# Kernel optimization log

Measured on AMD Instinct MI355X. Metric: run time of the kernel, lower is better.

## Reference

```python
import jax, jax.numpy as jnp
import numpy as np

N = 262144
FC = 256
XYZ_FREQ, DIR_FREQ = 10, 4
IN_XYZ = 3 + 3 * 2 * XYZ_FREQ  # 63
IN_DIR = 3 + 3 * 2 * DIR_FREQ  # 27
SKIP = 4


def posenc(p, n_freqs):
    bands = 2.0 ** jnp.arange(n_freqs, dtype=p.dtype)          # [F]
    xb = p[..., None, :] * bands[:, None]                       # [N, F, 3]
    sc = jnp.stack([jnp.sin(xb), jnp.cos(xb)], axis=-2)         # [N, F, 2, 3]
    return jnp.concatenate([p, sc.reshape(p.shape[0], n_freqs * 6)], axis=-1)


def setup_inputs() -> dict:
    key = jax.random.key(0)
    ks = jax.random.split(key, 32)
    s = 0.05
    inp = {"x": jax.random.normal(ks[0], (N, 6), jnp.float32)}
    dims_in = [IN_XYZ] + [FC + IN_XYZ if i == SKIP else FC for i in range(1, 8)]
    for i in range(8):
        inp[f"w{i}"] = jax.random.normal(ks[1 + i], (dims_in[i], FC), jnp.float32) * s
        inp[f"b{i}"] = jnp.zeros((FC,), jnp.float32)
    inp["w_final"] = jax.random.normal(ks[10], (FC, FC), jnp.float32) * s
    inp["b_final"] = jnp.zeros((FC,), jnp.float32)
    inp["w_sigma"] = jax.random.normal(ks[11], (FC, 1), jnp.float32) * s
    inp["b_sigma"] = jnp.zeros((1,), jnp.float32)
    inp["w_rgb1"] = jax.random.normal(ks[12], (FC + IN_DIR, FC // 2), jnp.float32) * s
    inp["b_rgb1"] = jnp.zeros((FC // 2,), jnp.float32)
    inp["w_rgb2"] = jax.random.normal(ks[13], (FC // 2, 3), jnp.float32) * s
    inp["b_rgb2"] = jnp.zeros((3,), jnp.float32)
    return inp


def reference(x, w0, b0, w1, b1, w2, b2, w3, b3, w4, b4, w5, b5, w6, b6, w7, b7,
              w_final, b_final, w_sigma, b_sigma, w_rgb1, b_rgb1, w_rgb2, b_rgb2):
    input_xyz = posenc(x[:, :3], XYZ_FREQ)   # [N, 63]
    input_dir = posenc(x[:, 3:], DIR_FREQ)   # [N, 27]
    ws = [w0, w1, w2, w3, w4, w5, w6, w7]
    bs = [b0, b1, b2, b3, b4, b5, b6, b7]
    h = input_xyz
    for i in range(8):
        if i == SKIP:
            h = jnp.concatenate([input_xyz, h], axis=-1)
        h = jax.nn.relu(h @ ws[i] + bs[i])
    sigma = h @ w_sigma + b_sigma                               # [N, 1]
    final = h @ w_final + b_final                               # [N, 256]
    dir_enc = jnp.concatenate([final, input_dir], axis=-1)      # [N, 283]
    hidden = jax.nn.relu(dir_enc @ w_rgb1 + b_rgb1)
    rgb = jax.nn.sigmoid(hidden @ w_rgb2 + b_rgb2)              # [N, 3]
    return jnp.concatenate([rgb, sigma], axis=-1)               # [N, 4]
```

## Files before the change

### kernel.cpp

```cpp
#include <hip/hip_runtime.h>
#include <hip/hip_fp16.h>
#include <stdint.h>

typedef unsigned int   uint32;
typedef unsigned short ushort_t;
typedef _Float16 half8   __attribute__((ext_vector_type(8)));
typedef float    floatx4 __attribute__((ext_vector_type(4)));

#define DEVINL __device__ __forceinline__

#define N_FRAGS 1172

DEVINL int fragoff(int row, int f) {
    return (f >> 5)*2048 + (row >> 4)*512 + ((f >> 3) & 3)*128 + (row & 15)*8 + (f & 7);
}

__device__ __align__(16) ushort_t g_ws[(size_t)N_FRAGS * 512];

DEVINL ushort_t f2h_u(float v) { return __half_as_ushort(__float2half(v)); }

DEVINL uint32 pk_relu(uint32 a) {
    uint32 r;
    asm("v_pk_max_f16 %0, %1, 0" : "=v"(r) : "v"(a));
    return r;
}

DEVINL void fast_sincos(float v, float& s, float& c) {
    float t = v * 0.15915494f;
    t = t - floorf(t);
    s = __builtin_amdgcn_sinf(t);
    c = __builtin_amdgcn_cosf(t);
}

__global__ __launch_bounds__(256) void prep_weights(
    const float* __restrict__ w0, const float* __restrict__ w1,
    const float* __restrict__ w2, const float* __restrict__ w3,
    const float* __restrict__ w4, const float* __restrict__ w5,
    const float* __restrict__ w6, const float* __restrict__ w7,
    const float* __restrict__ wf, const float* __restrict__ wsig,
    const float* __restrict__ wr1, const float* __restrict__ wr2)
{
    const int frag = blockIdx.x;
    const int w    = threadIdx.x;
    const int l    = w >> 2;
    const int jj   = w & 3;
    const int q = l >> 4, cc = l & 15;

    constexpr int foff[13] = {0,32,160,288,416,576,704,832,960,1088,1096,1168,1172};
    int t = 0;
    #pragma unroll
    for (int i = 1; i <= 11; ++i) if (frag >= foff[i]) t = i;

    const float* W; int fo, ntc, Kr, Nr;
    switch (t) {
        case 0:  W = w0;   fo = 0;    ntc = 16; Kr = 63;  Nr = 256; break;
        case 1:  W = w1;   fo = 32;   ntc = 16; Kr = 256; Nr = 256; break;
        case 2:  W = w2;   fo = 160;  ntc = 16; Kr = 256; Nr = 256; break;
        case 3:  W = w3;   fo = 288;  ntc = 16; Kr = 256; Nr = 256; break;
        case 4:  W = w4;   fo = 416;  ntc = 16; Kr = 319; Nr = 256; break;
        case 5:  W = w5;   fo = 576;  ntc = 16; Kr = 256; Nr = 256; break;
        case 6:  W = w6;   fo = 704;  ntc = 16; Kr = 256; Nr = 256; break;
        case 7:  W = w7;   fo = 832;  ntc = 16; Kr = 256; Nr = 256; break;
        case 8:  W = wf;   fo = 960;  ntc = 16; Kr = 256; Nr = 256; break;
        case 9:  W = wsig; fo = 1088; ntc = 1;  Kr = 256; Nr = 1;   break;
        case 10: W = wr1;  fo = 1096; ntc = 8;  Kr = 283; Nr = 128; break;
        default: W = wr2;  fo = 1168; ntc = 1;  Kr = 128; Nr = 3;   break;
    }
    const int skip63 = (t == 4);
    const int fl = frag - fo;
    const int nt = fl % ntc;
    const int kt = fl / ntc;
    const int n  = nt*16 + cc;

    ushort_t h2[2];
    #pragma unroll
    for (int e = 0; e < 2; ++e) {
        const int k = kt*32 + q*8 + jj*2 + e;
        float v = 0.f;
        if (n < Nr) {
            if (skip63) {
                if (k != 63) { const int rr = (k < 63) ? k : (k - 1); v = W[(size_t)rr*Nr + n]; }
            } else if (k < Kr) {
                v = W[(size_t)k*Nr + n];
            }
        }
        h2[e] = f2h_u(v);
    }
    const uint32 pk = (uint32)h2[0] | ((uint32)h2[1] << 16);
    ((uint32*)(g_ws + (size_t)frag*512))[l*4 + jj] = pk;
}

template <int NT_W, int KT, int KT_SPLIT, int NTT>
DEVINL void run_layer(const ushort_t* __restrict__ wsrc,
                      const ushort_t* __restrict__ in0,
                      const ushort_t* __restrict__ in1,
                      int lane, int nt_lo,
                      const floatx4 (&binit)[NT_W], floatx4 (&acc)[4][NT_W])
{
    half8 bfr[2][4];
    half8 afr[2][NT_W];

    const ushort_t* ap  = wsrc + (size_t)nt_lo*512 + (size_t)lane*8;
    const ushort_t* b0p = in0 + lane*8;
    const ushort_t* b1p = in1 + lane*8;

    auto loadA = [&](int kt, int buf) {
        const ushort_t* p = ap + (size_t)kt*NTT*512;
        #pragma unroll
        for (int nt = 0; nt < NT_W; ++nt)
            afr[buf][nt] = *(const half8*)(p + nt*512);
    };
    auto loadB = [&](int kt, int buf) {
        const ushort_t* bb = (kt < KT_SPLIT) ? b0p + kt*2048
                                             : b1p + (kt - KT_SPLIT)*2048;
        #pragma unroll
        for (int rt = 0; rt < 4; ++rt)
            bfr[buf][rt] = *(const half8*)(bb + rt*512);
    };

    loadA(0, 0);
    loadB(0, 0);
    #pragma unroll
    for (int kt = 0; kt < KT; ++kt) {
        const int cur = kt & 1;
        if (kt + 1 < KT) { loadA(kt + 1, cur ^ 1); loadB(kt + 1, cur ^ 1); }
        __builtin_amdgcn_s_setprio(1);
        #pragma unroll
        for (int nt = 0; nt < NT_W; ++nt)
            #pragma unroll
            for (int rt = 0; rt < 4; ++rt)
                acc[rt][nt] = __builtin_amdgcn_mfma_f32_16x16x32_f16(
                    afr[cur][nt], bfr[cur][rt],
                    (kt == 0) ? binit[nt] : acc[rt][nt], 0, 0, 0);
        __builtin_amdgcn_s_setprio(0);
    }
}

template <int NT_W, bool RELU>
DEVINL void epilogue_h(floatx4 (&acc)[4][NT_W], int nt_lo,
                       ushort_t* __restrict__ dsth, int q, int cc)
{
    ushort_t* base = dsth + (nt_lo >> 1)*2048 + (q >> 1)*128 + cc*8 + (q & 1)*4;
    #pragma unroll
    for (int rt = 0; rt < 4; ++rt) {
        #pragma unroll
        for (int nt = 0; nt < NT_W; ++nt) {
            const floatx4 v = acc[rt][nt];
            uint2 u;
            u.x = __builtin_bit_cast(uint32, __builtin_amdgcn_cvt_pkrtz(v.x, v.y));
            u.y = __builtin_bit_cast(uint32, __builtin_amdgcn_cvt_pkrtz(v.z, v.w));
            if (RELU) {
                u.x = pk_relu(u.x);
                u.y = pk_relu(u.y);
            }
            const int coff = (nt >> 1)*2048 + ((2*nt) & 3)*128 + rt*512;
            *(uint2*)(base + coff) = u;
        }
    }
}

__global__ __launch_bounds__(256, 3) void nerf_fused(
    const float* __restrict__ x,
    const float* __restrict__ b0, const float* __restrict__ b1,
    const float* __restrict__ b2, const float* __restrict__ b3,
    const float* __restrict__ b4, const float* __restrict__ b5,
    const float* __restrict__ b6, const float* __restrict__ b7,
    const float* __restrict__ bf, const float* __restrict__ bsig,
    const float* __restrict__ br1, const float* __restrict__ br2,
    float* __restrict__ out)
{
    __shared__ __align__(16) ushort_t shh[8*2048];
    __shared__ __align__(16) ushort_t shx[2*2048];
    __shared__ __align__(16) ushort_t shd[2048];

    const int tid  = threadIdx.x;
    const int wave = tid >> 6, lane = tid & 63;
    const int q = lane >> 4, cc = lane & 15;
    const int r0 = blockIdx.x * 64;
    const ushort_t* ws = g_ws;

    {
        const int r = lane;
        const float* xr = x + (size_t)(r0 + r)*6;
        for (int j = wave; j < 42; j += 4) {
            float s, c;
            if (j < 30) {
                int f = j/3, a = j%3;
                fast_sincos(xr[a] * (float)(1 << f), s, c);
                shx[fragoff(r, 3 + f*6 + a)]     = f2h_u(s);
                shx[fragoff(r, 3 + f*6 + 3 + a)] = f2h_u(c);
            } else {
                int jj = j - 30, f = jj/3, a = jj%3;
                fast_sincos(xr[3+a] * (float)(1 << f), s, c);
                shd[fragoff(r, 3 + f*6 + a)]     = f2h_u(s);
                shd[fragoff(r, 3 + f*6 + 3 + a)] = f2h_u(c);
            }
        }
        if (wave == 0) {
            #pragma unroll
            for (int a = 0; a < 3; ++a) {
                shx[fragoff(r, a)] = f2h_u(xr[a]);
                shd[fragoff(r, a)] = f2h_u(xr[3+a]);
            }
            shx[fragoff(r, 63)] = 0;
            #pragma unroll
            for (int kq = 27; kq < 32; ++kq) shd[fragoff(r, kq)] = 0;
        }
    }
    __syncthreads();

    const float* BS[8] = {b0,b1,b2,b3,b4,b5,b6,b7};
    const int WO[8] = {0,16384,81920,147456,212992,294912,360448,425984};
    const int nt_lo4 = wave * 4;
    const floatx4 vz = {0.f, 0.f, 0.f, 0.f};

    floatx4 acc[4][4];
    floatx4 bl[4];

    #pragma unroll
    for (int nt = 0; nt < 4; ++nt)
        bl[nt] = *(const floatx4*)(b0 + (nt_lo4 + nt)*16 + q*4);
    run_layer<4,2,2,16>(ws + WO[0], shx, shx, lane, nt_lo4, bl, acc);
    epilogue_h<4,true>(acc, nt_lo4, shh, q, cc);
    __syncthreads();

    #pragma unroll
    for (int l = 1; l < 8; ++l) {
        #pragma unroll
        for (int nt = 0; nt < 4; ++nt)
            bl[nt] = *(const floatx4*)(BS[l] + (nt_lo4 + nt)*16 + q*4);
        if (l == 4)
            run_layer<4,10,2,16>(ws + WO[4], shx, shh, lane, nt_lo4, bl, acc);
        else
            run_layer<4,8,8,16>(ws + WO[l], shh, shh, lane, nt_lo4, bl, acc);
        __syncthreads();
        epilogue_h<4,true>(acc, nt_lo4, shh, q, cc);
        __syncthreads();
    }

    if (wave == 0) {
        floatx4 sacc[4][1];
        const floatx4 bz[1] = {vz};
        run_layer<1,8,8,1>(ws + 557056, shh, shh, lane, 0, bz, sacc);
        if (q == 0) {
            const float bs_ = bsig[0];
            #pragma unroll
            for (int rt = 0; rt < 4; ++rt)
                out[(size_t)(r0 + rt*16 + cc)*4 + 3] = sacc[rt][0].x + bs_;
        }
    }

    #pragma unroll
    for (int nt = 0; nt < 4; ++nt)
        bl[nt] = *(const floatx4*)(bf + (nt_lo4 + nt)*16 + q*4);
    run_layer<4,8,8,16>(ws + 491520, shh, shh, lane, nt_lo4, bl, acc);
    __syncthreads();
    epilogue_h<4,false>(acc, nt_lo4, shh, q, cc);
    __syncthreads();

    {
        floatx4 racc[4][2];
        floatx4 bl2[2];
        #pragma unroll
        for (int nt = 0; nt < 2; ++nt)
            bl2[nt] = *(const floatx4*)(br1 + (wave*2 + nt)*16 + q*4);
        run_layer<2,9,8,8>(ws + 561152, shh, shd, lane, wave*2, bl2, racc);
        __syncthreads();
        epilogue_h<2,true>(racc, wave*2, shh, q, cc);
        __syncthreads();
    }

    if (wave == 0) {
        floatx4 cacc[4][1];
        const floatx4 bz[1] = {vz};
        run_layer<1,4,4,1>(ws + 598016, shh, shh, lane, 0, bz, cacc);
        if (q == 0) {
            const float c0 = br2[0], c1 = br2[1], c2 = br2[2];
            #pragma unroll
            for (int rt = 0; rt < 4; ++rt) {
                const size_t o = (size_t)(r0 + rt*16 + cc)*4;
                out[o+0] = 1.f/(1.f + __expf(-(cacc[rt][0].x + c0)));
                out[o+1] = 1.f/(1.f + __expf(-(cacc[rt][0].y + c1)));
                out[o+2] = 1.f/(1.f + __expf(-(cacc[rt][0].z + c2)));
            }
        }
    }
}

extern "C" void kernel_launch(void* const* d_in, const int* in_sizes, int n_in,
                              void* d_out, int out_size, void* d_ws, size_t ws_size,
                              hipStream_t stream)
{
    const float* x  = (const float*)d_in[0];
    const float* w0 = (const float*)d_in[1];  const float* b0 = (const float*)d_in[2];
    const float* w1 = (const float*)d_in[3];  const float* b1 = (const float*)d_in[4];
    const float* w2 = (const float*)d_in[5];  const float* b2 = (const float*)d_in[6];
    const float* w3 = (const float*)d_in[7];  const float* b3 = (const float*)d_in[8];
    const float* w4 = (const float*)d_in[9];  const float* b4 = (const float*)d_in[10];
    const float* w5 = (const float*)d_in[11]; const float* b5 = (const float*)d_in[12];
    const float* w6 = (const float*)d_in[13]; const float* b6 = (const float*)d_in[14];
    const float* w7 = (const float*)d_in[15]; const float* b7 = (const float*)d_in[16];
    const float* wf = (const float*)d_in[17]; const float* bf = (const float*)d_in[18];
    const float* wsg= (const float*)d_in[19]; const float* bsg= (const float*)d_in[20];
    const float* wr1= (const float*)d_in[21]; const float* br1= (const float*)d_in[22];
    const float* wr2= (const float*)d_in[23]; const float* br2= (const float*)d_in[24];
    float* out = (float*)d_out;
    const int N = in_sizes[0] / 6;

    prep_weights<<<N_FRAGS, 256, 0, stream>>>(
        w0,w1,w2,w3,w4,w5,w6,w7,wf,wsg,wr1,wr2);
    nerf_fused<<<N/64, 256, 0, stream>>>(
        x, b0,b1,b2,b3,b4,b5,b6,b7, bf,bsg, br1,br2, out);
}
```

Measured before the change: 365.5 us.

## Split each 64-row tile across 8 waves with two row groups

Doubles the block to 512 threads so that each wave computes 32 rows by 64 output columns instead of 64 by 64. This halves the accumulator registers per wave and should allow more waves in flight. The rgb1 layer is redistributed to give one 16-column tile per wave, and the epilogue gains a single-tile addressing path. The cost is that each weight fragment is now loaded from global memory by two waves instead of one, and block-wide barriers now synchronize 8 waves.

```diff
diff --git a/kernel.cpp b/kernel.cpp
--- a/kernel.cpp
+++ b/kernel.cpp
@@ -90,14 +90,14 @@
     ((uint32*)(g_ws + (size_t)frag*512))[l*4 + jj] = pk;
 }
 
-template <int NT_W, int KT, int KT_SPLIT, int NTT>
+template <int RT, int NT_W, int KT, int KT_SPLIT, int NTT>
 DEVINL void run_layer(const ushort_t* __restrict__ wsrc,
                       const ushort_t* __restrict__ in0,
                       const ushort_t* __restrict__ in1,
                       int lane, int nt_lo,
-                      const floatx4 (&binit)[NT_W], floatx4 (&acc)[4][NT_W])
-{
-    half8 bfr[2][4];
+                      const floatx4 (&binit)[NT_W], floatx4 (&acc)[RT][NT_W])
+{
+    half8 bfr[2][RT];
     half8 afr[2][NT_W];
 
     const ushort_t* ap  = wsrc + (size_t)nt_lo*512 + (size_t)lane*8;
@@ -114,7 +114,7 @@
         const ushort_t* bb = (kt < KT_SPLIT) ? b0p + kt*2048
                                              : b1p + (kt - KT_SPLIT)*2048;
         #pragma unroll
-        for (int rt = 0; rt < 4; ++rt)
+        for (int rt = 0; rt < RT; ++rt)
             bfr[buf][rt] = *(const half8*)(bb + rt*512);
     };
 
@@ -128,7 +128,7 @@
         #pragma unroll
         for (int nt = 0; nt < NT_W; ++nt)
             #pragma unroll
-            for (int rt = 0; rt < 4; ++rt)
+            for (int rt = 0; rt < RT; ++rt)
                 acc[rt][nt] = __builtin_amdgcn_mfma_f32_16x16x32_f16(
                     afr[cur][nt], bfr[cur][rt],
                     (kt == 0) ? binit[nt] : acc[rt][nt], 0, 0, 0);
@@ -136,13 +136,12 @@
     }
 }
 
-template <int NT_W, bool RELU>
-DEVINL void epilogue_h(floatx4 (&acc)[4][NT_W], int nt_lo,
+template <int RT, int NT_W, bool RELU>
+DEVINL void epilogue_h(floatx4 (&acc)[RT][NT_W], int nt_lo,
                        ushort_t* __restrict__ dsth, int q, int cc)
 {
-    ushort_t* base = dsth + (nt_lo >> 1)*2048 + (q >> 1)*128 + cc*8 + (q & 1)*4;
-    #pragma unroll
-    for (int rt = 0; rt < 4; ++rt) {
+    #pragma unroll
+    for (int rt = 0; rt < RT; ++rt) {
         #pragma unroll
         for (int nt = 0; nt < NT_W; ++nt) {
             const floatx4 v = acc[rt][nt];
@@ -153,13 +152,21 @@
                 u.x = pk_relu(u.x);
                 u.y = pk_relu(u.y);
             }
-            const int coff = (nt >> 1)*2048 + ((2*nt) & 3)*128 + rt*512;
-            *(uint2*)(base + coff) = u;
-        }
-    }
-}
-
-__global__ __launch_bounds__(256, 3) void nerf_fused(
+            int dst;
+            if constexpr (NT_W > 1) {
+                dst = (nt_lo >> 1)*2048 + (q >> 1)*128 + cc*8 + (q & 1)*4
+                    + (nt >> 1)*2048 + ((2*nt) & 3)*128 + rt*512;
+            } else {
+                const int ng = nt_lo + nt;
+                dst = (ng >> 1)*2048 + rt*512
+                    + (((2*ng + (q >> 1)) & 3)*16 + cc)*8 + (q & 1)*4;
+            }
+            *(uint2*)(dsth + dst) = u;
+        }
+    }
+}
+
+__global__ __launch_bounds__(512, 4) void nerf_fused(
     const float* __restrict__ x,
     const float* __restrict__ b0, const float* __restrict__ b1,
     const float* __restrict__ b2, const float* __restrict__ b3,
@@ -179,10 +186,15 @@
     const int r0 = blockIdx.x * 64;
     const ushort_t* ws = g_ws;
 
+    const int w4 = wave & 3;
+    const int rg = wave >> 2;
+    const int rgo = rg * 1024;
+    const int nt_lo4 = w4 * 4;
+
     {
         const int r = lane;
         const float* xr = x + (size_t)(r0 + r)*6;
-        for (int j = wave; j < 42; j += 4) {
+        for (int j = wave; j < 42; j += 8) {
             float s, c;
             if (j < 30) {
                 int f = j/3, a = j%3;
@@ -211,17 +223,16 @@
 
     const float* BS[8] = {b0,b1,b2,b3,b4,b5,b6,b7};
     const int WO[8] = {0,16384,81920,147456,212992,294912,360448,425984};
-    const int nt_lo4 = wave * 4;
     const floatx4 vz = {0.f, 0.f, 0.f, 0.f};
 
-    floatx4 acc[4][4];
+    floatx4 acc[2][4];
     floatx4 bl[4];
 
     #pragma unroll
     for (int nt = 0; nt < 4; ++nt)
         bl[nt] = *(const floatx4*)(b0 + (nt_lo4 + nt)*16 + q*4);
-    run_layer<4,2,2,16>(ws + WO[0], shx, shx, lane, nt_lo4, bl, acc);
-    epilogue_h<4,true>(acc, nt_lo4, shh, q, cc);
+    run_layer<2,4,2,2,16>(ws + WO[0], shx + rgo, shx + rgo, lane, nt_lo4, bl, acc);
+    epilogue_h<2,4,true>(acc, nt_lo4, shh + rgo, q, cc);
     __syncthreads();
 
     #pragma unroll
@@ -230,18 +241,18 @@
         for (int nt = 0; nt < 4; ++nt)
             bl[nt] = *(const floatx4*)(BS[l] + (nt_lo4 + nt)*16 + q*4);
         if (l == 4)
-            run_layer<4,10,2,16>(ws + WO[4], shx, shh, lane, nt_lo4, bl, acc);
+            run_layer<2,4,10,2,16>(ws + WO[4], shx + rgo, shh + rgo, lane, nt_lo4, bl, acc);
         else
-            run_layer<4,8,8,16>(ws + WO[l], shh, shh, lane, nt_lo4, bl, acc);
+            run_layer<2,4,8,8,16>(ws + WO[l], shh + rgo, shh + rgo, lane, nt_lo4, bl, acc);
         __syncthreads();
-        epilogue_h<4,true>(acc, nt_lo4, shh, q, cc);
+        epilogue_h<2,4,true>(acc, nt_lo4, shh + rgo, q, cc);
         __syncthreads();
     }
 
     if (wave == 0) {
         floatx4 sacc[4][1];
         const floatx4 bz[1] = {vz};
-        run_layer<1,8,8,1>(ws + 557056, shh, shh, lane, 0, bz, sacc);
+        run_layer<4,1,8,8,1>(ws + 557056, shh, shh, lane, 0, bz, sacc);
         if (q == 0) {
             const float bs_ = bsig[0];
             #pragma unroll
@@ -253,27 +264,25 @@
     #pragma unroll
     for (int nt = 0; nt < 4; ++nt)
         bl[nt] = *(const floatx4*)(bf + (nt_lo4 + nt)*16 + q*4);
-    run_layer<4,8,8,16>(ws + 491520, shh, shh, lane, nt_lo4, bl, acc);
+    run_layer<2,4,8,8,16>(ws + 491520, shh + rgo, shh + rgo, lane, nt_lo4, bl, acc);
     __syncthreads();
-    epilogue_h<4,false>(acc, nt_lo4, shh, q, cc);
+    epilogue_h<2,4,false>(acc, nt_lo4, shh + rgo, q, cc);
     __syncthreads();
 
     {
-        floatx4 racc[4][2];
-        floatx4 bl2[2];
-        #pragma unroll
-        for (int nt = 0; nt < 2; ++nt)
-            bl2[nt] = *(const floatx4*)(br1 + (wave*2 + nt)*16 + q*4);
-        run_layer<2,9,8,8>(ws + 561152, shh, shd, lane, wave*2, bl2, racc);
+        floatx4 racc[4][1];
+        floatx4 bl2[1];
+        bl2[0] = *(const floatx4*)(br1 + wave*16 + q*4);
+        run_layer<4,1,9,8,8>(ws + 561152, shh, shd, lane, wave, bl2, racc);
         __syncthreads();
-        epilogue_h<2,true>(racc, wave*2, shh, q, cc);
+        epilogue_h<4,1,true>(racc, wave, shh, q, cc);
         __syncthreads();
     }
 
     if (wave == 0) {
         floatx4 cacc[4][1];
         const floatx4 bz[1] = {vz};
-        run_layer<1,4,4,1>(ws + 598016, shh, shh, lane, 0, bz, cacc);
+        run_layer<4,1,4,4,1>(ws + 598016, shh, shh, lane, 0, bz, cacc);
         if (q == 0) {
             const float c0 = br2[0], c1 = br2[1], c2 = br2[2];
             #pragma unroll
@@ -309,6 +318,6 @@
 
     prep_weights<<<N_FRAGS, 256, 0, stream>>>(
         w0,w1,w2,w3,w4,w5,w6,w7,wf,wsg,wr1,wr2);
-    nerf_fused<<<N/64, 256, 0, stream>>>(
+    nerf_fused<<<N/64, 512, 0, stream>>>(
         x, b0,b1,b2,b3,b4,b5,b6,b7, bf,bsg, br1,br2, out);
 }
```

New measurement: 468.4 us. 28.1% more time.

## Drop register double-buffering and alias direction encoding into xyz LDS to raise occupancy

Applied to the files above, without the earlier changes.

Removes the double-buffered A/B fragment registers in the MFMA layer loop, so each k-step loads and then computes. Alongside this it raises launch bounds from 3 to 4 blocks per CU. It also drops the separate direction-encoding LDS buffer by reusing the xyz encoding buffer after layer 4 (the last layer that reads it), recomputing the direction posenc there. The aim is lower VGPR and LDS use to fit more blocks per CU, at the cost of exposing load latency inside the k-loop and doing extra posenc work mid-network.

```diff
diff --git a/kernel.cpp b/kernel.cpp
--- a/kernel.cpp
+++ b/kernel.cpp
@@ -97,40 +97,31 @@
                       int lane, int nt_lo,
                       const floatx4 (&binit)[NT_W], floatx4 (&acc)[4][NT_W])
 {
-    half8 bfr[2][4];
-    half8 afr[2][NT_W];
+    half8 bfr[4];
+    half8 afr[NT_W];
 
     const ushort_t* ap  = wsrc + (size_t)nt_lo*512 + (size_t)lane*8;
     const ushort_t* b0p = in0 + lane*8;
     const ushort_t* b1p = in1 + lane*8;
 
-    auto loadA = [&](int kt, int buf) {
+    #pragma unroll
+    for (int kt = 0; kt < KT; ++kt) {
         const ushort_t* p = ap + (size_t)kt*NTT*512;
         #pragma unroll
         for (int nt = 0; nt < NT_W; ++nt)
-            afr[buf][nt] = *(const half8*)(p + nt*512);
-    };
-    auto loadB = [&](int kt, int buf) {
+            afr[nt] = *(const half8*)(p + nt*512);
         const ushort_t* bb = (kt < KT_SPLIT) ? b0p + kt*2048
                                              : b1p + (kt - KT_SPLIT)*2048;
         #pragma unroll
         for (int rt = 0; rt < 4; ++rt)
-            bfr[buf][rt] = *(const half8*)(bb + rt*512);
-    };
-
-    loadA(0, 0);
-    loadB(0, 0);
-    #pragma unroll
-    for (int kt = 0; kt < KT; ++kt) {
-        const int cur = kt & 1;
-        if (kt + 1 < KT) { loadA(kt + 1, cur ^ 1); loadB(kt + 1, cur ^ 1); }
+            bfr[rt] = *(const half8*)(bb + rt*512);
         __builtin_amdgcn_s_setprio(1);
         #pragma unroll
         for (int nt = 0; nt < NT_W; ++nt)
             #pragma unroll
             for (int rt = 0; rt < 4; ++rt)
                 acc[rt][nt] = __builtin_amdgcn_mfma_f32_16x16x32_f16(
-                    afr[cur][nt], bfr[cur][rt],
+                    afr[nt], bfr[rt],
                     (kt == 0) ? binit[nt] : acc[rt][nt], 0, 0, 0);
         __builtin_amdgcn_s_setprio(0);
     }
@@ -159,7 +150,7 @@
     }
 }
 
-__global__ __launch_bounds__(256, 3) void nerf_fused(
+__global__ __launch_bounds__(256, 4) void nerf_fused(
     const float* __restrict__ x,
     const float* __restrict__ b0, const float* __restrict__ b1,
     const float* __restrict__ b2, const float* __restrict__ b3,
@@ -171,7 +162,7 @@
 {
     __shared__ __align__(16) ushort_t shh[8*2048];
     __shared__ __align__(16) ushort_t shx[2*2048];
-    __shared__ __align__(16) ushort_t shd[2048];
+    ushort_t* shd = shx;
 
     const int tid  = threadIdx.x;
     const int wave = tid >> 6, lane = tid & 63;
@@ -182,29 +173,17 @@
     {
         const int r = lane;
         const float* xr = x + (size_t)(r0 + r)*6;
-        for (int j = wave; j < 42; j += 4) {
+        for (int j = wave; j < 30; j += 4) {
             float s, c;
-            if (j < 30) {
-                int f = j/3, a = j%3;
-                fast_sincos(xr[a] * (float)(1 << f), s, c);
-                shx[fragoff(r, 3 + f*6 + a)]     = f2h_u(s);
-                shx[fragoff(r, 3 + f*6 + 3 + a)] = f2h_u(c);
-            } else {
-                int jj = j - 30, f = jj/3, a = jj%3;
-                fast_sincos(xr[3+a] * (float)(1 << f), s, c);
-                shd[fragoff(r, 3 + f*6 + a)]     = f2h_u(s);
-                shd[fragoff(r, 3 + f*6 + 3 + a)] = f2h_u(c);
-            }
+            int f = j/3, a = j%3;
+            fast_sincos(xr[a] * (float)(1 << f), s, c);
+            shx[fragoff(r, 3 + f*6 + a)]     = f2h_u(s);
+            shx[fragoff(r, 3 + f*6 + 3 + a)] = f2h_u(c);
         }
         if (wave == 0) {
             #pragma unroll
-            for (int a = 0; a < 3; ++a) {
-                shx[fragoff(r, a)] = f2h_u(xr[a]);
-                shd[fragoff(r, a)] = f2h_u(xr[3+a]);
-            }
+            for (int a = 0; a < 3; ++a) shx[fragoff(r, a)] = f2h_u(xr[a]);
             shx[fragoff(r, 63)] = 0;
-            #pragma unroll
-            for (int kq = 27; kq < 32; ++kq) shd[fragoff(r, kq)] = 0;
         }
     }
     __syncthreads();
@@ -234,6 +213,23 @@
         else
             run_layer<4,8,8,16>(ws + WO[l], shh, shh, lane, nt_lo4, bl, acc);
         __syncthreads();
+        if (l == 4) {
+            const int r = lane;
+            const float* xr = x + (size_t)(r0 + r)*6;
+            for (int j = wave; j < 12; j += 4) {
+                float s, c;
+                int f = j/3, a = j%3;
+                fast_sincos(xr[3+a] * (float)(1 << f), s, c);
+                shd[fragoff(r, 3 + f*6 + a)]     = f2h_u(s);
+                shd[fragoff(r, 3 + f*6 + 3 + a)] = f2h_u(c);
+            }
+            if (wave == 0) {
+                #pragma unroll
+                for (int a = 0; a < 3; ++a) shd[fragoff(r, a)] = f2h_u(xr[3+a]);
+                #pragma unroll
+                for (int kq = 27; kq < 32; ++kq) shd[fragoff(r, kq)] = 0;
+            }
+        }
         epilogue_h<4,true>(acc, nt_lo4, shh, q, cc);
         __syncthreads();
     }
```

Measured after the change: 369.7 us. About the same (+1.1%).
